# Kernel tuning notes

Measured on AMD Instinct MI355X. Metric: run time of the kernel, lower is better.

Reference implementation:

```python
import jax, jax.numpy as jnp
import numpy as np

XSIZE = 128
B = 8
N = 262144


def setup_inputs() -> dict:
    key = jax.random.key(0)
    k1, k2 = jax.random.split(key)
    indices = jax.random.randint(k1, (B, N, 3), 0, XSIZE, dtype=jnp.int32)
    values = jax.random.normal(k2, (B, N), dtype=jnp.float32)
    return {"indices": indices, "values": values, "xsize": XSIZE}


def reference(indices, values, xsize):
    # Batched equivalent of tf.map_fn(tensor_scatter_nd_add) per sample:
    # scatter-add N point values into a zero (xsize, xsize, xsize) grid.
    def build_grid(idx, val):
        grid = jnp.zeros((xsize, xsize, xsize), dtype=val.dtype)
        return grid.at[idx[:, 0], idx[:, 1], idx[:, 2]].add(val)

    grid = jax.vmap(build_grid)(indices, values)  # [B, X, X, X]

    # Adjacent-voxel differences along each spatial axis
    d1 = grid[:, 1:, :, :] - grid[:, :-1, :, :]
    d2 = grid[:, :, 1:, :] - grid[:, :, :-1, :]
    d3 = grid[:, :, :, 1:] - grid[:, :, :, :-1]

    ax = (1, 2, 3)
    # Total variation loss: sum |diff| / num_voxels (xsize^3)
    num_voxels = jnp.float32(xsize * xsize * xsize)
    tv = (jnp.sum(jnp.abs(d1), axis=ax)
          + jnp.sum(jnp.abs(d2), axis=ax)
          + jnp.sum(jnp.abs(d3), axis=ax)) / num_voxels

    # MSE smoothness loss: sum diff^2 / (2*xsize^2 - 2*xsize)
    # (faithful to TF code, which uses only shape[1:3] for the denominator)
    num_pairs = jnp.float32(2 * xsize * xsize - 2 * xsize)
    mse = (jnp.sum(jnp.square(d1), axis=ax)
           + jnp.sum(jnp.square(d2), axis=ax)
           + jnp.sum(jnp.square(d3), axis=ax)) / num_pairs

    return tv, mse
```

## Files before the change

kernel.cpp:

```cpp
#include <hip/hip_runtime.h>
#include <hip/hip_fp16.h>

constexpr unsigned XS        = 128;
constexpr unsigned NB        = 8;
constexpr unsigned NPTS      = 262144;
constexpr unsigned TOTAL_PTS = NB * NPTS;
constexpr unsigned PPB       = 4096;
constexpr unsigned NSEG      = TOTAL_PTS / PPB;
constexpr unsigned NBKT      = NB * XS;
constexpr unsigned CAP       = 3072;
constexpr unsigned GSTRIDE   = 16;

constexpr size_t REC2_U32 = (size_t)NBKT * CAP;

__global__ __launch_bounds__(512) void bin_kernel(
        const int* __restrict__ idx, const float* __restrict__ vals,
        unsigned* __restrict__ rec2, unsigned* __restrict__ gcur) {
    __shared__ unsigned long long sbuf[PPB];
    __shared__ unsigned hist[XS], cur[XS], loff[XS], gbase[XS];
    unsigned tid = threadIdx.x, g = blockIdx.x;
    unsigned b = g >> 6;
    unsigned base = g * PPB;

    if (tid < XS) hist[tid] = 0u;

    unsigned key[8]; float val[8];
    const unsigned* ibuf = (const unsigned*)sbuf;
    for (unsigned r = 0; r < 2u; ++r) {
        __syncthreads();
        {
            const uint4* src = (const uint4*)idx + ((size_t)g * 3072u + r * 1536u);
            uint4* dst = (uint4*)sbuf;
#pragma unroll
            for (unsigned n = 0; n < 3u; ++n) dst[n * 512u + tid] = src[n * 512u + tid];
        }
        __syncthreads();
#pragma unroll
        for (unsigned n = 0; n < 4u; ++n) {
            unsigned p = n * 512u + tid;
            unsigned i = ibuf[3u * p], j = ibuf[3u * p + 1u], k = ibuf[3u * p + 2u];
            unsigned m = r * 4u + n;
            key[m] = (i << 14) | (j << 7) | k;
            val[m] = vals[base + r * 2048u + p];
            atomicAdd(&hist[i], 1u);
        }
    }
    __syncthreads();

    if (tid < 64u) {
        unsigned h0 = hist[tid], h1 = hist[64u + tid];
        unsigned a0 = h0, a1 = h1;
#pragma unroll
        for (unsigned o = 1; o <= 32; o <<= 1) {
            unsigned t0 = __shfl_up(a0, o, 64);
            unsigned t1 = __shfl_up(a1, o, 64);
            if (tid >= o) { a0 += t0; a1 += t1; }
        }
        a1 += __shfl(a0, 63, 64);
        unsigned e0 = a0 - h0, e1 = a1 - h1;
        loff[tid] = e0; loff[64u + tid] = e1;
        cur[tid]  = e0; cur[64u + tid]  = e1;
    }
    __syncthreads();
    if (tid < XS)
        gbase[tid] = atomicAdd(&gcur[(b * XS + tid) * GSTRIDE], hist[tid]);

#pragma unroll
    for (unsigned m = 0; m < 8u; ++m) {
        unsigned i = key[m] >> 14;
        unsigned pos = atomicAdd(&cur[i], 1u);
        sbuf[pos] = ((unsigned long long)__float_as_uint(val[m]) << 32)
                  | (unsigned long long)key[m];
    }
    __syncthreads();

#pragma unroll
    for (unsigned m = 0; m < 8u; ++m) {
        unsigned s = m * 512u + tid;
        unsigned long long rr = sbuf[s];
        unsigned bin = ((unsigned)rr >> 14) & 127u;
        unsigned dst = gbase[bin] + (s - loff[bin]);
        unsigned short hv = __half_as_ushort(
            __float2half(__uint_as_float((unsigned)(rr >> 32))));
        if (dst < CAP)
            __builtin_nontemporal_store(
                ((unsigned)hv << 16) | ((unsigned)rr & 0x3FFFu),
                &rec2[(size_t)(b * XS + bin) * CAP + dst]);
    }
}

__global__ __launch_bounds__(512) void accum_kernel(
        const unsigned* __restrict__ rec2,
        const unsigned* __restrict__ gcur, float* __restrict__ stage) {
    __shared__ float strip[65u * XS];
    __shared__ float sred[16];
    unsigned z = blockIdx.x;
    unsigned b = z >> 7, i = z & 127u;
    bool has_d1 = (i < 127u);
    unsigned tid = threadIdx.x, lane = tid & 63u, w = tid >> 6;

    unsigned cnt0 = min(gcur[(b * XS + i) * GSTRIDE], CAP);
    unsigned cnt1 = has_d1 ? min(gcur[(b * XS + i + 1u) * GSTRIDE], CAP) : 0u;
    const unsigned long long* bA =
        (const unsigned long long*)(rec2 + (size_t)(b * XS + i) * CAP);
    const unsigned long long* bB =
        (const unsigned long long*)(rec2 + (size_t)(b * XS + i + 1u) * CAP);

    unsigned long long rvA[3]; bool avA[3];
    unsigned long long rvB[3]; bool avB[3];
#pragma unroll
    for (unsigned q = 0; q < 3u; ++q) {
        unsigned r2 = q * 512u + tid;
        avA[q] = (2u * r2) < cnt0;
        if (avA[q]) rvA[q] = __builtin_nontemporal_load(bA + r2);
    }
#pragma unroll
    for (unsigned q = 0; q < 3u; ++q) {
        unsigned r2 = q * 512u + tid;
        avB[q] = has_d1 && (2u * r2) < cnt1;
        if (avB[q]) rvB[q] = __builtin_nontemporal_load(bB + r2);
    }

    float tvb = 0.f, mseb = 0.f;
    for (unsigned t = 0; t < 2u; ++t) {
        unsigned j0 = t << 6;
        auto process = [&](unsigned rc, float sg, unsigned lmax) {
            unsigned l = ((rc >> 7) & 127u) - j0;
            if (l <= lmax)
                atomicAdd(&strip[(l << 7) | (rc & 127u)],
                          sg * __half2float(__ushort_as_half((unsigned short)(rc >> 16))));
        };

        __syncthreads();
        float4* p4 = (float4*)strip;
        for (unsigned r = tid; r < 2080u; r += 512u)
            p4[r] = float4{0.f, 0.f, 0.f, 0.f};
        __syncthreads();

#pragma unroll
        for (unsigned q = 0; q < 3u; ++q)
            if (avA[q]) {
                unsigned r0 = 2u * (q * 512u + tid);
                process((unsigned)rvA[q], 1.f, 64u);
                if (r0 + 1u < cnt0) process((unsigned)(rvA[q] >> 32), 1.f, 64u);
            }
        __syncthreads();

        unsigned jmax = 127u - j0;
        float tv = 0.f, mse = 0.f;
#pragma unroll
        for (unsigned r = 0; r < 4u; ++r) {
            unsigned v4 = r * 512u + tid;
            unsigned l = v4 >> 5, k4 = v4 & 31u;
            float4 c = p4[v4];
            float d0 = c.y - c.x, d1 = c.z - c.y, d2 = c.w - c.z;
            tv  += fabsf(d0) + fabsf(d1) + fabsf(d2);
            mse += d0 * d0 + d1 * d1 + d2 * d2;
            if (k4 < 31u) {
                float nx = strip[(v4 << 2) + 4u];
                float d3 = nx - c.w;
                tv += fabsf(d3); mse += d3 * d3;
            }
            if (l < jmax) {
                float4 n = p4[v4 + 32u];
                float e0 = n.x - c.x, e1 = n.y - c.y, e2 = n.z - c.z, e3 = n.w - c.w;
                tv  += fabsf(e0) + fabsf(e1) + fabsf(e2) + fabsf(e3);
                mse += e0 * e0 + e1 * e1 + e2 * e2 + e3 * e3;
            }
        }

        if (has_d1) {
            __syncthreads();
#pragma unroll
            for (unsigned q = 0; q < 3u; ++q)
                if (avB[q]) {
                    unsigned r0 = 2u * (q * 512u + tid);
                    process((unsigned)rvB[q], -1.f, 63u);
                    if (r0 + 1u < cnt1) process((unsigned)(rvB[q] >> 32), -1.f, 63u);
                }
            __syncthreads();
#pragma unroll
            for (unsigned r = 0; r < 4u; ++r) {
                float4 dd = p4[r * 512u + tid];
                tv  += fabsf(dd.x) + fabsf(dd.y) + fabsf(dd.z) + fabsf(dd.w);
                mse += dd.x * dd.x + dd.y * dd.y + dd.z * dd.z + dd.w * dd.w;
            }
        }
        tvb += tv; mseb += mse;
    }

#pragma unroll
    for (int o = 32; o > 0; o >>= 1) {
        tvb  += __shfl_down(tvb, o, 64);
        mseb += __shfl_down(mseb, o, 64);
    }
    if (lane == 0u) { sred[w] = tvb; sred[8u + w] = mseb; }
    __syncthreads();
    if (tid == 0u) {
        float tt = 0.f, mm = 0.f;
#pragma unroll
        for (unsigned q = 0; q < 8u; ++q) { tt += sred[q]; mm += sred[8u + q]; }
        atomicAdd(stage + (size_t)b * 16u,        tt);
        atomicAdd(stage + (size_t)(8u + b) * 16u, mm);
    }
}

__global__ void finalize_kernel(const float* __restrict__ stage,
                                float* __restrict__ out) {
    unsigned i = threadIdx.x;
    if (i < 16u) {
        float s = stage[i * 16u];
        float scale = (i < 8u) ? (1.0f / 2097152.0f)
                               : (1.0f / 32512.0f);
        out[i] = s * scale;
    }
}

extern "C" void kernel_launch(void* const* d_in, const int* in_sizes, int n_in,
                              void* d_out, int out_size, void* d_ws, size_t ws_size,
                              hipStream_t stream) {
    const int*   idx  = (const int*)d_in[0];
    const float* vals = (const float*)d_in[1];

    unsigned* rec2  = (unsigned*)d_ws;
    unsigned* gcur  = rec2 + REC2_U32;
    float*    stage = (float*)(gcur + (size_t)NBKT * GSTRIDE);
    float*    out   = (float*)d_out;

    (void)hipMemsetAsync(gcur, 0, (size_t)NBKT * GSTRIDE * 4 + 256 * 4, stream);

    bin_kernel<<<NSEG, 512, 0, stream>>>(idx, vals, rec2, gcur);
    accum_kernel<<<NBKT, 512, 0, stream>>>(rec2, gcur, stage);
    finalize_kernel<<<1, 64, 0, stream>>>(stage, out);
}
```

Measured before the change: 114.9 us.

## Use full-plane LDS accumulation with 1024 threads and direct index loads

The accumulation kernel now holds a whole 128x128 plane (64 KB of LDS) per block with 1024 threads, replacing the two-pass half-plane strip loop. Each record is scattered once rather than filtered twice, which removes the redundant passes and half the barriers. The binning kernel now reads index triples straight from global memory with strided scalar loads instead of staging them through LDS with coalesced uint4 copies. This trades coalescing for fewer syncs, and the larger LDS footprint lowers the number of resident blocks per CU.

```diff
diff --git a/kernel.cpp b/kernel.cpp
--- a/kernel.cpp
+++ b/kernel.cpp
@@ -10,8 +10,8 @@
 constexpr unsigned NBKT      = NB * XS;
 constexpr unsigned CAP       = 3072;
 constexpr unsigned GSTRIDE   = 16;
-
-constexpr size_t REC2_U32 = (size_t)NBKT * CAP;
+constexpr size_t   REC2_U32  = (size_t)NBKT * CAP;
+
 
 __global__ __launch_bounds__(512) void bin_kernel(
         const int* __restrict__ idx, const float* __restrict__ vals,
@@ -23,27 +23,17 @@
     unsigned base = g * PPB;
 
     if (tid < XS) hist[tid] = 0u;
+    __syncthreads();
 
     unsigned key[8]; float val[8];
-    const unsigned* ibuf = (const unsigned*)sbuf;
-    for (unsigned r = 0; r < 2u; ++r) {
-        __syncthreads();
-        {
-            const uint4* src = (const uint4*)idx + ((size_t)g * 3072u + r * 1536u);
-            uint4* dst = (uint4*)sbuf;
-#pragma unroll
-            for (unsigned n = 0; n < 3u; ++n) dst[n * 512u + tid] = src[n * 512u + tid];
-        }
-        __syncthreads();
-#pragma unroll
-        for (unsigned n = 0; n < 4u; ++n) {
-            unsigned p = n * 512u + tid;
-            unsigned i = ibuf[3u * p], j = ibuf[3u * p + 1u], k = ibuf[3u * p + 2u];
-            unsigned m = r * 4u + n;
-            key[m] = (i << 14) | (j << 7) | k;
-            val[m] = vals[base + r * 2048u + p];
-            atomicAdd(&hist[i], 1u);
-        }
+#pragma unroll
+    for (unsigned m = 0; m < 8u; ++m) {
+        unsigned p = m * 512u + tid;
+        const int* t = idx + (size_t)(base + p) * 3u;
+        unsigned i = (unsigned)t[0], j = (unsigned)t[1], k = (unsigned)t[2];
+        key[m] = (i << 14) | (j << 7) | k;
+        val[m] = vals[base + p];
+        atomicAdd(&hist[i], 1u);
     }
     __syncthreads();
 
@@ -89,11 +79,11 @@
     }
 }
 
-__global__ __launch_bounds__(512) void accum_kernel(
+__global__ __launch_bounds__(1024, 8) void accum_kernel(
         const unsigned* __restrict__ rec2,
         const unsigned* __restrict__ gcur, float* __restrict__ stage) {
-    __shared__ float strip[65u * XS];
-    __shared__ float sred[16];
+    __shared__ float plane[XS * XS];
+    __shared__ float sred[32];
     unsigned z = blockIdx.x;
     unsigned b = z >> 7, i = z & 127u;
     bool has_d1 = (i < 127u);
@@ -106,100 +96,97 @@
     const unsigned long long* bB =
         (const unsigned long long*)(rec2 + (size_t)(b * XS + i + 1u) * CAP);
 
-    unsigned long long rvA[3]; bool avA[3];
-    unsigned long long rvB[3]; bool avB[3];
-#pragma unroll
-    for (unsigned q = 0; q < 3u; ++q) {
-        unsigned r2 = q * 512u + tid;
-        avA[q] = (2u * r2) < cnt0;
+    unsigned long long rvA[2], rvB[2]; bool avA[2], avB[2];
+#pragma unroll
+    for (unsigned q = 0; q < 2u; ++q) {
+        unsigned r2 = q * 1024u + tid;
+        avA[q] = (r2 < 1536u) && (2u * r2) < cnt0;
         if (avA[q]) rvA[q] = __builtin_nontemporal_load(bA + r2);
-    }
-#pragma unroll
-    for (unsigned q = 0; q < 3u; ++q) {
-        unsigned r2 = q * 512u + tid;
-        avB[q] = has_d1 && (2u * r2) < cnt1;
+        avB[q] = has_d1 && (r2 < 1536u) && (2u * r2) < cnt1;
         if (avB[q]) rvB[q] = __builtin_nontemporal_load(bB + r2);
     }
 
-    float tvb = 0.f, mseb = 0.f;
-    for (unsigned t = 0; t < 2u; ++t) {
-        unsigned j0 = t << 6;
-        auto process = [&](unsigned rc, float sg, unsigned lmax) {
-            unsigned l = ((rc >> 7) & 127u) - j0;
-            if (l <= lmax)
-                atomicAdd(&strip[(l << 7) | (rc & 127u)],
-                          sg * __half2float(__ushort_as_half((unsigned short)(rc >> 16))));
-        };
-
+    float4* p4 = (float4*)plane;
+#pragma unroll
+    for (unsigned v = 0; v < 4u; ++v) p4[v * 1024u + tid] = float4{0.f, 0.f, 0.f, 0.f};
+    __syncthreads();
+
+#pragma unroll
+    for (unsigned q = 0; q < 2u; ++q)
+        if (avA[q]) {
+            unsigned r0 = 2u * (q * 1024u + tid);
+            {
+                unsigned rc = (unsigned)rvA[q];
+                atomicAdd(&plane[rc & 16383u],
+                          __half2float(__ushort_as_half((unsigned short)(rc >> 16))));
+            }
+            if (r0 + 1u < cnt0) {
+                unsigned rc = (unsigned)(rvA[q] >> 32);
+                atomicAdd(&plane[rc & 16383u],
+                          __half2float(__ushort_as_half((unsigned short)(rc >> 16))));
+            }
+        }
+    __syncthreads();
+
+    float tv = 0.f, mse = 0.f;
+#pragma unroll
+    for (unsigned n = 0; n < 4u; ++n) {
+        unsigned v4 = n * 1024u + tid;
+        unsigned l = v4 >> 5, k4 = v4 & 31u;
+        float4 c = p4[v4];
+        float d0 = c.y - c.x, d1v = c.z - c.y, d2v = c.w - c.z;
+        tv  += fabsf(d0) + fabsf(d1v) + fabsf(d2v);
+        mse += d0 * d0 + d1v * d1v + d2v * d2v;
+        if (k4 < 31u) {
+            float nx = plane[(v4 << 2) + 4u];
+            float d3 = nx - c.w;
+            tv += fabsf(d3); mse += d3 * d3;
+        }
+        if (l < 127u) {
+            float4 nr = p4[v4 + 32u];
+            float e0 = nr.x - c.x, e1 = nr.y - c.y, e2 = nr.z - c.z, e3 = nr.w - c.w;
+            tv  += fabsf(e0) + fabsf(e1) + fabsf(e2) + fabsf(e3);
+            mse += e0 * e0 + e1 * e1 + e2 * e2 + e3 * e3;
+        }
+    }
+
+    if (has_d1) {
         __syncthreads();
-        float4* p4 = (float4*)strip;
-        for (unsigned r = tid; r < 2080u; r += 512u)
-            p4[r] = float4{0.f, 0.f, 0.f, 0.f};
-        __syncthreads();
-
-#pragma unroll
-        for (unsigned q = 0; q < 3u; ++q)
-            if (avA[q]) {
-                unsigned r0 = 2u * (q * 512u + tid);
-                process((unsigned)rvA[q], 1.f, 64u);
-                if (r0 + 1u < cnt0) process((unsigned)(rvA[q] >> 32), 1.f, 64u);
+#pragma unroll
+        for (unsigned q = 0; q < 2u; ++q)
+            if (avB[q]) {
+                unsigned r0 = 2u * (q * 1024u + tid);
+                {
+                    unsigned rc = (unsigned)rvB[q];
+                    atomicAdd(&plane[rc & 16383u],
+                              -__half2float(__ushort_as_half((unsigned short)(rc >> 16))));
+                }
+                if (r0 + 1u < cnt1) {
+                    unsigned rc = (unsigned)(rvB[q] >> 32);
+                    atomicAdd(&plane[rc & 16383u],
+                              -__half2float(__ushort_as_half((unsigned short)(rc >> 16))));
+                }
             }
         __syncthreads();
-
-        unsigned jmax = 127u - j0;
-        float tv = 0.f, mse = 0.f;
-#pragma unroll
-        for (unsigned r = 0; r < 4u; ++r) {
-            unsigned v4 = r * 512u + tid;
-            unsigned l = v4 >> 5, k4 = v4 & 31u;
-            float4 c = p4[v4];
-            float d0 = c.y - c.x, d1 = c.z - c.y, d2 = c.w - c.z;
-            tv  += fabsf(d0) + fabsf(d1) + fabsf(d2);
-            mse += d0 * d0 + d1 * d1 + d2 * d2;
-            if (k4 < 31u) {
-                float nx = strip[(v4 << 2) + 4u];
-                float d3 = nx - c.w;
-                tv += fabsf(d3); mse += d3 * d3;
-            }
-            if (l < jmax) {
-                float4 n = p4[v4 + 32u];
-                float e0 = n.x - c.x, e1 = n.y - c.y, e2 = n.z - c.z, e3 = n.w - c.w;
-                tv  += fabsf(e0) + fabsf(e1) + fabsf(e2) + fabsf(e3);
-                mse += e0 * e0 + e1 * e1 + e2 * e2 + e3 * e3;
-            }
-        }
-
-        if (has_d1) {
-            __syncthreads();
-#pragma unroll
-            for (unsigned q = 0; q < 3u; ++q)
-                if (avB[q]) {
-                    unsigned r0 = 2u * (q * 512u + tid);
-                    process((unsigned)rvB[q], -1.f, 63u);
-                    if (r0 + 1u < cnt1) process((unsigned)(rvB[q] >> 32), -1.f, 63u);
-                }
-            __syncthreads();
-#pragma unroll
-            for (unsigned r = 0; r < 4u; ++r) {
-                float4 dd = p4[r * 512u + tid];
-                tv  += fabsf(dd.x) + fabsf(dd.y) + fabsf(dd.z) + fabsf(dd.w);
-                mse += dd.x * dd.x + dd.y * dd.y + dd.z * dd.z + dd.w * dd.w;
-            }
-        }
-        tvb += tv; mseb += mse;
+#pragma unroll
+        for (unsigned n = 0; n < 4u; ++n) {
+            float4 dd = p4[n * 1024u + tid];
+            tv  += fabsf(dd.x) + fabsf(dd.y) + fabsf(dd.z) + fabsf(dd.w);
+            mse += dd.x * dd.x + dd.y * dd.y + dd.z * dd.z + dd.w * dd.w;
+        }
     }
 
 #pragma unroll
     for (int o = 32; o > 0; o >>= 1) {
-        tvb  += __shfl_down(tvb, o, 64);
-        mseb += __shfl_down(mseb, o, 64);
-    }
-    if (lane == 0u) { sred[w] = tvb; sred[8u + w] = mseb; }
+        tv  += __shfl_down(tv, o, 64);
+        mse += __shfl_down(mse, o, 64);
+    }
+    if (lane == 0u) { sred[w] = tv; sred[16u + w] = mse; }
     __syncthreads();
     if (tid == 0u) {
         float tt = 0.f, mm = 0.f;
 #pragma unroll
-        for (unsigned q = 0; q < 8u; ++q) { tt += sred[q]; mm += sred[8u + q]; }
+        for (unsigned q = 0; q < 16u; ++q) { tt += sred[q]; mm += sred[16u + q]; }
         atomicAdd(stage + (size_t)b * 16u,        tt);
         atomicAdd(stage + (size_t)(8u + b) * 16u, mm);
     }
@@ -230,6 +217,6 @@
     (void)hipMemsetAsync(gcur, 0, (size_t)NBKT * GSTRIDE * 4 + 256 * 4, stream);
 
     bin_kernel<<<NSEG, 512, 0, stream>>>(idx, vals, rec2, gcur);
-    accum_kernel<<<NBKT, 512, 0, stream>>>(rec2, gcur, stage);
+    accum_kernel<<<NBKT, 1024, 0, stream>>>(rec2, gcur, stage);
     finalize_kernel<<<1, 64, 0, stream>>>(stage, out);
 }
```

New measurement: 117.8 us. +2.5%, slower.
